# Kernel optimization log

Hardware: AMD Instinct MI355X
Metric: run time of the kernel (lower is better)

Reference implementation:

```python
import math
import jax, jax.numpy as jnp
import numpy as np

B, S, D = 2, 2048, 512
H = 8
DPH = D // H
NEG = -1e18


def lorentz_linear(x, W, b, log_scale):
    """LorentzLinear with head_num=H: linear map then per-head projection onto the
    Lorentz hyperboloid: time = sigmoid(y0)*exp(scale)+1.1, space rescaled so that
    -time^2 + |space|^2 = -1 per head chunk."""
    Bx, Sx, Dx = x.shape
    y = (x @ W.T + b).reshape(Bx, Sx, H, DPH)
    time = jax.nn.sigmoid(y[..., :1]) * jnp.exp(log_scale) + 1.1
    space = y[..., 1:]
    sq = jnp.clip(jnp.sum(space * space, axis=-1, keepdims=True), 1e-8, None)
    scale = (time * time - 1.0) / sq
    out = jnp.concatenate([time, space * jnp.sqrt(scale)], axis=-1)
    return out.reshape(Bx, Sx, Dx)


def setup_inputs() -> dict:
    key0 = jax.random.key(0)
    ks = jax.random.split(key0, 8)
    std = 1.0 / np.sqrt(D)
    causal = ~jnp.tril(jnp.ones((S, S), dtype=bool))  # True = masked out
    return {
        "key": jax.random.normal(ks[0], (B, S, D), jnp.float32),
        "value": jax.random.normal(ks[1], (B, S, D), jnp.float32),
        "query": jax.random.normal(ks[2], (B, S, D), jnp.float32),
        "mask": jnp.broadcast_to(causal[None], (B, S, S)),
        "Wq": jax.random.normal(ks[3], (D, D), jnp.float32) * std,
        "bq": jnp.zeros((D,), jnp.float32),
        "sq": jnp.asarray(math.log(10.0), jnp.float32),
        "Wk": jax.random.normal(ks[4], (D, D), jnp.float32) * std,
        "bk": jnp.zeros((D,), jnp.float32),
        "sk": jnp.asarray(math.log(10.0), jnp.float32),
        "Wv": jax.random.normal(ks[5], (D, D), jnp.float32) * std,
        "bv": jnp.zeros((D,), jnp.float32),
        "sv": jnp.asarray(math.log(10.0), jnp.float32),
        "att_scale": jnp.full((1,), math.sqrt(D), jnp.float32),
        "att_bias": jnp.zeros((), jnp.float32),
    }


def reference(key, value, query, mask, Wq, bq, sq, Wk, bk, sk, Wv, bv, sv,
              att_scale, att_bias):
    def shape(x):  # (B,S,D) -> (B,H,S,dph)
        return x.reshape(B, -1, H, DPH).transpose(0, 2, 1, 3)

    q = shape(lorentz_linear(query, Wq, bq, sq))
    k = shape(lorentz_linear(key, Wk, bk, sk))
    v = shape(lorentz_linear(value, Wv, bv, sv))

    # Lorentz inner product <q,k>_L = -q0*k0 + q_space . k_space
    qm = jnp.concatenate([-q[..., :1], q[..., 1:]], axis=-1)
    cin = jnp.einsum('bhqd,bhkd->bhqk', qm, k)
    scores = (2.0 + 2.0 * cin) / att_scale + att_bias
    scores = jnp.where(mask[:, None], NEG, scores)
    attn = jax.nn.softmax(scores, axis=-1)  # (B,H,Q,K)

    # mid_point: weighted mean then renormalize to the hyperboloid
    ave = jnp.einsum('bhqk,bhkd->bhqd', attn, v)
    inner = -ave[..., :1] ** 2 + jnp.sum(ave[..., 1:] ** 2, axis=-1, keepdims=True)
    denom = jnp.sqrt(jnp.clip(jnp.abs(-inner), 1e-8, None))
    context = (ave / denom).transpose(0, 2, 1, 3)  # (B,Q,H,dph)
    return context, attn
```

## Files before the change

### kernel.cpp

```cpp
#include <hip/hip_runtime.h>
#include <math.h>

#define BB 2
#define SS 2048
#define DD 512
#define HH 8
#define MM (BB*SS)
#define CTX_ELEMS (MM*DD)

typedef __attribute__((ext_vector_type(8))) __bf16 bf16x8;
typedef __attribute__((ext_vector_type(4))) float  f32x4;

static __device__ inline unsigned short f2bf(float x) {
    unsigned u = __builtin_bit_cast(unsigned, x);
    u += 0x7fffu + ((u >> 16) & 1u);
    return (unsigned short)(u >> 16);
}
static __device__ inline float bf2f(unsigned short h) {
    unsigned u = ((unsigned)h) << 16;
    return __builtin_bit_cast(float, u);
}

static __device__ inline void unpack8(const uint4& a, const uint4& b, bf16x8& h, bf16x8& l) {
    uint4 hu, lu;
    hu.x = __builtin_amdgcn_perm(a.y, a.x, 0x05040100u);
    hu.y = __builtin_amdgcn_perm(a.w, a.z, 0x05040100u);
    hu.z = __builtin_amdgcn_perm(b.y, b.x, 0x05040100u);
    hu.w = __builtin_amdgcn_perm(b.w, b.z, 0x05040100u);
    lu.x = __builtin_amdgcn_perm(a.y, a.x, 0x07060302u);
    lu.y = __builtin_amdgcn_perm(a.w, a.z, 0x07060302u);
    lu.z = __builtin_amdgcn_perm(b.y, b.x, 0x07060302u);
    lu.w = __builtin_amdgcn_perm(b.w, b.z, 0x07060302u);
    h = __builtin_bit_cast(bf16x8, hu);
    l = __builtin_bit_cast(bf16x8, lu);
}

__global__ __launch_bounds__(256)
void lorentz_proj_kernel(const float* __restrict__ Xq, const float* __restrict__ Xk, const float* __restrict__ Xv,
                         const float* __restrict__ Wq, const float* __restrict__ bq, const float* __restrict__ sq,
                         const float* __restrict__ Wk, const float* __restrict__ bk, const float* __restrict__ sk,
                         const float* __restrict__ Wv, const float* __restrict__ bv, const float* __restrict__ sv,
                         float* __restrict__ oq, float* __restrict__ ok_, float* __restrict__ ov)
{
    __shared__ float smem[8704];
    float* Xs = smem;
    float* Ws = smem + 4224;

    const float* X; const float* W; const float* bias; const float* ls; float* out;
    if (blockIdx.z == 0)      { X = Xq; W = Wq; bias = bq; ls = sq; out = oq;  }
    else if (blockIdx.z == 1) { X = Xk; W = Wk; bias = bk; ls = sk; out = ok_; }
    else                      { X = Xv; W = Wv; bias = bv; ls = sv; out = ov;  }

    const int tid = threadIdx.x;
    const int tx = tid & 15, ty = tid >> 4;
    const int m0 = blockIdx.x << 7;
    const int n0 = blockIdx.y << 7;

    float acc[8][8];
#pragma unroll
    for (int i = 0; i < 8; ++i)
#pragma unroll
        for (int j = 0; j < 8; ++j) acc[i][j] = 0.f;

    const int lrow = tid >> 3;
    const int lk   = (tid & 7) << 2;

    for (int k0 = 0; k0 < DD; k0 += 32) {
        __syncthreads();
#pragma unroll
        for (int r = 0; r < 4; ++r) {
            const int row = lrow + (r << 5);
            const float4 xv = *(const float4*)(X + (size_t)(m0 + row) * DD + k0 + lk);
            const float4 wv = *(const float4*)(W + (size_t)(n0 + row) * DD + k0 + lk);
            Xs[(lk+0)*132 + row] = xv.x; Xs[(lk+1)*132 + row] = xv.y;
            Xs[(lk+2)*132 + row] = xv.z; Xs[(lk+3)*132 + row] = xv.w;
            Ws[(lk+0)*132 + row] = wv.x; Ws[(lk+1)*132 + row] = wv.y;
            Ws[(lk+2)*132 + row] = wv.z; Ws[(lk+3)*132 + row] = wv.w;
        }
        __syncthreads();
#pragma unroll
        for (int k = 0; k < 32; ++k) {
            const float4 a0 = *(const float4*)(Xs + k*132 + (ty << 3));
            const float4 a1 = *(const float4*)(Xs + k*132 + (ty << 3) + 4);
            const float4 b0 = *(const float4*)(Ws + k*132 + (tx << 3));
            const float4 b1 = *(const float4*)(Ws + k*132 + (tx << 3) + 4);
            const float av[8] = {a0.x,a0.y,a0.z,a0.w,a1.x,a1.y,a1.z,a1.w};
            const float bw[8] = {b0.x,b0.y,b0.z,b0.w,b1.x,b1.y,b1.z,b1.w};
#pragma unroll
            for (int i = 0; i < 8; ++i)
#pragma unroll
                for (int j = 0; j < 8; ++j)
                    acc[i][j] = fmaf(av[i], bw[j], acc[i][j]);
        }
    }

    const float es = expf(ls[0]);

#pragma unroll
    for (int half = 0; half < 2; ++half) {
        __syncthreads();
        if ((tx >> 3) == half) {
            const int cx = tx & 7;
#pragma unroll
            for (int i = 0; i < 8; ++i) {
                const int row = (ty << 3) + i;
#pragma unroll
                for (int j = 0; j < 8; ++j) {
                    const int cih = (cx << 3) + j;
                    smem[row*68 + cih] = acc[i][j] + bias[n0 + (half << 6) + cih];
                }
            }
        }
        __syncthreads();
        const int row = tid >> 1;
        const int t2  = tid & 1;
        float ssum = 0.f;
        for (int j = 1 + t2; j < 64; j += 2) {
            const float v = smem[row*68 + j];
            ssum = fmaf(v, v, ssum);
        }
        ssum += __shfl_xor(ssum, 1);
        const float y0  = smem[row*68];
        const float tim = es / (1.f + expf(-y0)) + 1.1f;
        const float scf = sqrtf((tim*tim - 1.f) / fmaxf(ssum, 1e-8f));
        const int g = m0 + row;
        const int b = g >> 11;
        const int s = g & (SS - 1);
        const int h = (n0 >> 6) + half;
        float* op = out + ((size_t)(b*HH + h)*SS + s) * 64;
        if (t2 == 0) op[0] = tim;
        for (int j = 1 + t2; j < 64; j += 2) op[j] = smem[row*68 + j] * scf;
    }
}

__global__ __launch_bounds__(256)
void lorentz_attn_mfma(const float* __restrict__ qws, const float* __restrict__ kws, const float* __restrict__ vws,
                       const float* __restrict__ att_scale, const float* __restrict__ att_bias,
                       float* __restrict__ ctx, float* __restrict__ attn)
{
    __shared__ __align__(16) char sm[49152];
    char* Kh = sm;
    char* Kl = sm + 8192;
    char* Vp = sm + 16384;
    char* Pp = sm + 32768;
    char* Qh = Pp;
    char* Ql = Pp + 8192;

    const int tid = threadIdx.x;
    const int bh  = blockIdx.y;
    const int qt  = (bh >= 8) ? blockIdx.x : (31 - blockIdx.x);
    const int l63 = tid & 63;
    const int w   = tid >> 6;
    const int qoff = (w >> 1) << 5;
    const int joff = (w & 1) << 5;
    const int lg  = l63 >> 4;
    const int ll  = l63 & 15;

    const float inv_s = 1.f / att_scale[0];
    const float c1 = 2.f * inv_s;
    const float c0 = 2.f * inv_s + att_bias[0];

    const float* qb = qws + (size_t)bh * SS * 64;
    const float* kb = kws + (size_t)bh * SS * 64;
    const float* vb = vws + (size_t)bh * SS * 64;

    const int jr = tid >> 4;
    const int d0 = (tid & 15) << 2;

#pragma unroll
    for (int r = 0; r < 4; ++r) {
        const int j = jr + (r << 4);
        float4 x = *(const float4*)(qb + (size_t)(qt*64 + j)*64 + d0);
        if (d0 == 0) x.x = -x.x;
        const unsigned short h0=f2bf(x.x), h1=f2bf(x.y), h2=f2bf(x.z), h3=f2bf(x.w);
        ushort4 hv = {h0,h1,h2,h3};
        ushort4 lv = {f2bf(x.x-bf2f(h0)), f2bf(x.y-bf2f(h1)), f2bf(x.z-bf2f(h2)), f2bf(x.w-bf2f(h3))};
        const int byte = ((j<<7) + (d0<<1)) ^ ((j&7)<<4);
        *(ushort4*)(Qh + byte) = hv;
        *(ushort4*)(Ql + byte) = lv;
    }
    __syncthreads();

    bf16x8 qh[2][2], ql[2][2];
#pragma unroll
    for (int m = 0; m < 2; ++m)
#pragma unroll
        for (int dc = 0; dc < 2; ++dc) {
            const int q = qoff + (m<<4) + ll;
            const int byte = ((q<<7) + (dc<<6) + (lg<<4)) ^ ((q&7)<<4);
            qh[m][dc] = *(const bf16x8*)(Qh + byte);
            ql[m][dc] = *(const bf16x8*)(Ql + byte);
        }
    __syncthreads();

    float lrow[2][4] = {{0.f,0.f,0.f,0.f},{0.f,0.f,0.f,0.f}};

    for (int jt = 0; jt <= qt; ++jt) {
        __syncthreads();
#pragma unroll
        for (int r = 0; r < 4; ++r) {
            const int j = jr + (r << 4);
            const float4 x = *(const float4*)(kb + (size_t)(jt*64 + j)*64 + d0);
            const unsigned short h0=f2bf(x.x), h1=f2bf(x.y), h2=f2bf(x.z), h3=f2bf(x.w);
            ushort4 hv = {h0,h1,h2,h3};
            ushort4 lv = {f2bf(x.x-bf2f(h0)), f2bf(x.y-bf2f(h1)), f2bf(x.z-bf2f(h2)), f2bf(x.w-bf2f(h3))};
            const int byte = ((j<<7) + (d0<<1)) ^ ((j&7)<<4);
            *(ushort4*)(Kh + byte) = hv;
            *(ushort4*)(Kl + byte) = lv;
        }
        __syncthreads();

        f32x4 sacc[2][2];
#pragma unroll
        for (int m = 0; m < 2; ++m)
#pragma unroll
            for (int n = 0; n < 2; ++n) sacc[m][n] = (f32x4){0.f,0.f,0.f,0.f};
#pragma unroll
        for (int dc = 0; dc < 2; ++dc) {
            bf16x8 kh[2], kl[2];
#pragma unroll
            for (int n = 0; n < 2; ++n) {
                const int j = joff + (n<<4) + ll;
                const int byte = ((j<<7) + (dc<<6) + (lg<<4)) ^ ((j&7)<<4);
                kh[n] = *(const bf16x8*)(Kh + byte);
                kl[n] = *(const bf16x8*)(Kl + byte);
            }
#pragma unroll
            for (int m = 0; m < 2; ++m)
#pragma unroll
                for (int n = 0; n < 2; ++n) {
                    sacc[m][n] = __builtin_amdgcn_mfma_f32_16x16x32_bf16(qh[m][dc], kh[n], sacc[m][n], 0,0,0);
                    sacc[m][n] = __builtin_amdgcn_mfma_f32_16x16x32_bf16(qh[m][dc], kl[n], sacc[m][n], 0,0,0);
                    sacc[m][n] = __builtin_amdgcn_mfma_f32_16x16x32_bf16(ql[m][dc], kh[n], sacc[m][n], 0,0,0);
                }
        }

        const bool diag = (jt == qt);
#pragma unroll
        for (int m = 0; m < 2; ++m)
#pragma unroll
            for (int reg = 0; reg < 4; ++reg) {
                const int ri = qoff + (m<<4) + (lg<<2) + reg;
                float rs = 0.f;
#pragma unroll
                for (int n = 0; n < 2; ++n) {
                    const int cj = joff + (n<<4) + ll;
                    const float sc = sacc[m][n][reg] * c1 + c0;
                    rs += (!diag || cj <= ri) ? __expf(sc) : 0.f;
                }
                rs += __shfl_xor(rs, 1); rs += __shfl_xor(rs, 2);
                rs += __shfl_xor(rs, 4); rs += __shfl_xor(rs, 8);
                lrow[m][reg] += rs;
            }
    }

    __syncthreads();
    {
        float* dred = (float*)sm;
        if (ll == 0) {
#pragma unroll
            for (int m = 0; m < 2; ++m)
#pragma unroll
                for (int reg = 0; reg < 4; ++reg)
                    dred[(qoff + (m<<4) + (lg<<2) + reg)*2 + (w & 1)] = lrow[m][reg];
        }
        __syncthreads();
#pragma unroll
        for (int m = 0; m < 2; ++m)
#pragma unroll
            for (int reg = 0; reg < 4; ++reg) {
                const int ri = qoff + (m<<4) + (lg<<2) + reg;
                lrow[m][reg] = dred[ri*2] + dred[ri*2 + 1];
            }
    }

    float il[2][4];
#pragma unroll
    for (int m = 0; m < 2; ++m)
#pragma unroll
        for (int reg = 0; reg < 4; ++reg) il[m][reg] = 1.f / lrow[m][reg];

    f32x4 oacc[2][2];
#pragma unroll
    for (int m = 0; m < 2; ++m)
#pragma unroll
        for (int n = 0; n < 2; ++n) oacc[m][n] = (f32x4){0.f,0.f,0.f,0.f};

    for (int jt = 0; jt <= qt; ++jt) {
        __syncthreads();
#pragma unroll
        for (int r = 0; r < 4; ++r) {
            const int j = jr + (r << 4);
            const float4 x = *(const float4*)(kb + (size_t)(jt*64 + j)*64 + d0);
            const unsigned short h0=f2bf(x.x), h1=f2bf(x.y), h2=f2bf(x.z), h3=f2bf(x.w);
            ushort4 hv = {h0,h1,h2,h3};
            ushort4 lv = {f2bf(x.x-bf2f(h0)), f2bf(x.y-bf2f(h1)), f2bf(x.z-bf2f(h2)), f2bf(x.w-bf2f(h3))};
            const int byte = ((j<<7) + (d0<<1)) ^ ((j&7)<<4);
            *(ushort4*)(Kh + byte) = hv;
            *(ushort4*)(Kl + byte) = lv;

            const float4 v = *(const float4*)(vb + (size_t)(jt*64 + j)*64 + d0);
            const float vs[4] = {v.x, v.y, v.z, v.w};
#pragma unroll
            for (int c = 0; c < 4; ++c) {
                const int d = d0 + c;
                const unsigned short vh = f2bf(vs[c]);
                const unsigned short vlo = f2bf(vs[c] - bf2f(vh));
                const int vbyte = ((d<<8) + (j<<2)) ^ ((d&7)<<4);
                *(unsigned*)(Vp + vbyte) = (unsigned)vh | ((unsigned)vlo << 16);
            }
        }
        __syncthreads();

        f32x4 sacc[2][2];
#pragma unroll
        for (int m = 0; m < 2; ++m)
#pragma unroll
            for (int n = 0; n < 2; ++n) sacc[m][n] = (f32x4){0.f,0.f,0.f,0.f};
#pragma unroll
        for (int dc = 0; dc < 2; ++dc) {
            bf16x8 kh[2], kl[2];
#pragma unroll
            for (int n = 0; n < 2; ++n) {
                const int j = joff + (n<<4) + ll;
                const int byte = ((j<<7) + (dc<<6) + (lg<<4)) ^ ((j&7)<<4);
                kh[n] = *(const bf16x8*)(Kh + byte);
                kl[n] = *(const bf16x8*)(Kl + byte);
            }
#pragma unroll
            for (int m = 0; m < 2; ++m)
#pragma unroll
                for (int n = 0; n < 2; ++n) {
                    sacc[m][n] = __builtin_amdgcn_mfma_f32_16x16x32_bf16(qh[m][dc], kh[n], sacc[m][n], 0,0,0);
                    sacc[m][n] = __builtin_amdgcn_mfma_f32_16x16x32_bf16(qh[m][dc], kl[n], sacc[m][n], 0,0,0);
                    sacc[m][n] = __builtin_amdgcn_mfma_f32_16x16x32_bf16(ql[m][dc], kh[n], sacc[m][n], 0,0,0);
                }
        }

        const bool diag = (jt == qt);
#pragma unroll
        for (int m = 0; m < 2; ++m)
#pragma unroll
            for (int reg = 0; reg < 4; ++reg) {
                const int ri = qoff + (m<<4) + (lg<<2) + reg;
                const int gi = (qt<<6) + ri;
#pragma unroll
                for (int n = 0; n < 2; ++n) {
                    const int cj = joff + (n<<4) + ll;
                    const float sc = sacc[m][n][reg] * c1 + c0;
                    const float p = (!diag || cj <= ri) ? __expf(sc) : 0.f;
                    const float pn = p * il[m][reg];
                    attn[((size_t)bh*SS + gi)*SS + (jt<<6) + cj] = pn;
                    const unsigned short ph = f2bf(pn);
                    const unsigned short pl = f2bf(pn - bf2f(ph));
                    const int byte = ((ri<<8) + (cj<<2)) ^ ((ri&7)<<4);
                    *(unsigned*)(Pp + byte) = (unsigned)ph | ((unsigned)pl << 16);
                }
            }
        __syncthreads();

#pragma unroll
        for (int jc = 0; jc < 2; ++jc) {
            bf16x8 pah[2], pal[2], vfh[2], vfl[2];
            const int jbase4 = ((jc<<5) + (lg<<3)) << 2;
#pragma unroll
            for (int m = 0; m < 2; ++m) {
                const int q = qoff + (m<<4) + ll;
                const int X = (q<<8) + jbase4;
                const int s = (q&7)<<4;
                const uint4 a = *(const uint4*)(Pp + (X ^ s));
                const uint4 b = *(const uint4*)(Pp + ((X + 16) ^ s));
                unpack8(a, b, pah[m], pal[m]);
            }
#pragma unroll
            for (int n = 0; n < 2; ++n) {
                const int d = joff + (n<<4) + ll;
                const int X = (d<<8) + jbase4;
                const int s = (d&7)<<4;
                const uint4 a = *(const uint4*)(Vp + (X ^ s));
                const uint4 b = *(const uint4*)(Vp + ((X + 16) ^ s));
                unpack8(a, b, vfh[n], vfl[n]);
            }
#pragma unroll
            for (int m = 0; m < 2; ++m)
#pragma unroll
                for (int n = 0; n < 2; ++n) {
                    oacc[m][n] = __builtin_amdgcn_mfma_f32_16x16x32_bf16(pah[m], vfh[n], oacc[m][n], 0,0,0);
                    oacc[m][n] = __builtin_amdgcn_mfma_f32_16x16x32_bf16(pah[m], vfl[n], oacc[m][n], 0,0,0);
                    oacc[m][n] = __builtin_amdgcn_mfma_f32_16x16x32_bf16(pal[m], vfh[n], oacc[m][n], 0,0,0);
                }
        }
    }

    {
        const int cstart = (qt + 1) << 6;
        const float4 z = make_float4(0.f, 0.f, 0.f, 0.f);
        for (int r = 0; r < 64; ++r) {
            float* rowp = attn + ((size_t)bh*SS + (qt<<6) + r)*SS;
            for (int c = cstart + (tid << 2); c < SS; c += 1024)
                *(float4*)(rowp + c) = z;
        }
    }

    float part[2][4];
#pragma unroll
    for (int m = 0; m < 2; ++m)
#pragma unroll
        for (int reg = 0; reg < 4; ++reg) {
            float s = 0.f;
#pragma unroll
            for (int n = 0; n < 2; ++n) {
                const int d = joff + (n<<4) + ll;
                const float av = oacc[m][n][reg] * il[m][reg];
                s += (d == 0) ? -av*av : av*av;
            }
            s += __shfl_xor(s, 1); s += __shfl_xor(s, 2);
            s += __shfl_xor(s, 4); s += __shfl_xor(s, 8);
            part[m][reg] = s;
        }
    __syncthreads();
    float* red = (float*)sm;
    if (ll == 0) {
#pragma unroll
        for (int m = 0; m < 2; ++m)
#pragma unroll
            for (int reg = 0; reg < 4; ++reg)
                red[(qoff + (m<<4) + (lg<<2) + reg)*2 + (w & 1)] = part[m][reg];
    }
    __syncthreads();

    const int b = bh >> 3, h = bh & 7;
#pragma unroll
    for (int m = 0; m < 2; ++m)
#pragma unroll
        for (int reg = 0; reg < 4; ++reg) {
            const int ri = qoff + (m<<4) + (lg<<2) + reg;
            const float inner = red[ri*2] + red[ri*2 + 1];
            const float dinv = 1.f / sqrtf(fmaxf(fabsf(inner), 1e-8f));
            const int gi = (qt<<6) + ri;
#pragma unroll
            for (int n = 0; n < 2; ++n) {
                const int d = joff + (n<<4) + ll;
                const float av = oacc[m][n][reg] * il[m][reg];
                ctx[((size_t)(b*SS + gi)*HH + h)*64 + d] = av * dinv;
            }
        }
}

extern "C" void kernel_launch(void* const* d_in, const int* in_sizes, int n_in,
                              void* d_out, int out_size, void* d_ws, size_t ws_size,
                              hipStream_t stream)
{
    const float* key   = (const float*)d_in[0];
    const float* value = (const float*)d_in[1];
    const float* query = (const float*)d_in[2];
    const float* Wq = (const float*)d_in[4];
    const float* bq = (const float*)d_in[5];
    const float* sq = (const float*)d_in[6];
    const float* Wk = (const float*)d_in[7];
    const float* bk = (const float*)d_in[8];
    const float* sk = (const float*)d_in[9];
    const float* Wv = (const float*)d_in[10];
    const float* bv = (const float*)d_in[11];
    const float* sv = (const float*)d_in[12];
    const float* as_ = (const float*)d_in[13];
    const float* ab  = (const float*)d_in[14];

    float* ws  = (float*)d_ws;
    float* qws = ws;
    float* kws = ws + (size_t)CTX_ELEMS;
    float* vws = ws + (size_t)2 * CTX_ELEMS;

    float* ctx  = (float*)d_out;
    float* attn = ctx + (size_t)CTX_ELEMS;

    dim3 pgrid(MM / 128, DD / 128, 3);
    lorentz_proj_kernel<<<pgrid, 256, 0, stream>>>(query, key, value,
                                                   Wq, bq, sq, Wk, bk, sk, Wv, bv, sv,
                                                   qws, kws, vws);

    dim3 agrid(32, BB * HH);
    lorentz_attn_mfma<<<agrid, 256, 0, stream>>>(qws, kws, vws, as_, ab, ctx, attn);
}
```

Measured before the change: 598.7 us.

## Port Lorentz projection GEMM to bf16x3 MFMA with register-level head normalization

Replaces the FP32 FMA tiled projection GEMM with MFMA 16x16x32 bf16 instructions. Each operand is split into high and low bf16 parts and three products are accumulated to keep near-FP32 accuracy. Tiles are stored in XOR-swizzled shared memory. The hyperboloid normalization epilogue now works directly on the MFMA accumulators, using wave shuffles for the per-head norm instead of a shared-memory staging pass. The tradeoff is extra conversion work, higher shared-memory use (64KB) and a small loss of precision compared with true FP32.

```diff
diff --git a/kernel.cpp b/kernel.cpp
--- a/kernel.cpp
+++ b/kernel.cpp
@@ -36,15 +36,17 @@
 }
 
 __global__ __launch_bounds__(256)
-void lorentz_proj_kernel(const float* __restrict__ Xq, const float* __restrict__ Xk, const float* __restrict__ Xv,
-                         const float* __restrict__ Wq, const float* __restrict__ bq, const float* __restrict__ sq,
-                         const float* __restrict__ Wk, const float* __restrict__ bk, const float* __restrict__ sk,
-                         const float* __restrict__ Wv, const float* __restrict__ bv, const float* __restrict__ sv,
-                         float* __restrict__ oq, float* __restrict__ ok_, float* __restrict__ ov)
+void lorentz_proj_mfma(const float* __restrict__ Xq, const float* __restrict__ Xk, const float* __restrict__ Xv,
+                       const float* __restrict__ Wq, const float* __restrict__ bq, const float* __restrict__ sq,
+                       const float* __restrict__ Wk, const float* __restrict__ bk, const float* __restrict__ sk,
+                       const float* __restrict__ Wv, const float* __restrict__ bv, const float* __restrict__ sv,
+                       float* __restrict__ oq, float* __restrict__ ok_, float* __restrict__ ov)
 {
-    __shared__ float smem[8704];
-    float* Xs = smem;
-    float* Ws = smem + 4224;
+    __shared__ __align__(16) char sm[65536];
+    char* Ah = sm;
+    char* Al = sm + 16384;
+    char* Bh = sm + 32768;
+    char* Bl = sm + 49152;
 
     const float* X; const float* W; const float* bias; const float* ls; float* out;
     if (blockIdx.z == 0)      { X = Xq; W = Wq; bias = bq; ls = sq; out = oq;  }
@@ -52,84 +54,112 @@
     else                      { X = Xv; W = Wv; bias = bv; ls = sv; out = ov;  }
 
     const int tid = threadIdx.x;
-    const int tx = tid & 15, ty = tid >> 4;
+    const int l63 = tid & 63;
+    const int w   = tid >> 6;
+    const int wm  = w >> 1;
+    const int wn  = w & 1;
+    const int lg  = l63 >> 4;
+    const int ll  = l63 & 15;
+
     const int m0 = blockIdx.x << 7;
     const int n0 = blockIdx.y << 7;
 
-    float acc[8][8];
-#pragma unroll
-    for (int i = 0; i < 8; ++i)
-#pragma unroll
-        for (int j = 0; j < 8; ++j) acc[i][j] = 0.f;
-
-    const int lrow = tid >> 3;
-    const int lk   = (tid & 7) << 2;
-
-    for (int k0 = 0; k0 < DD; k0 += 32) {
-        __syncthreads();
-#pragma unroll
-        for (int r = 0; r < 4; ++r) {
-            const int row = lrow + (r << 5);
-            const float4 xv = *(const float4*)(X + (size_t)(m0 + row) * DD + k0 + lk);
-            const float4 wv = *(const float4*)(W + (size_t)(n0 + row) * DD + k0 + lk);
-            Xs[(lk+0)*132 + row] = xv.x; Xs[(lk+1)*132 + row] = xv.y;
-            Xs[(lk+2)*132 + row] = xv.z; Xs[(lk+3)*132 + row] = xv.w;
-            Ws[(lk+0)*132 + row] = wv.x; Ws[(lk+1)*132 + row] = wv.y;
-            Ws[(lk+2)*132 + row] = wv.z; Ws[(lk+3)*132 + row] = wv.w;
-        }
-        __syncthreads();
-#pragma unroll
-        for (int k = 0; k < 32; ++k) {
-            const float4 a0 = *(const float4*)(Xs + k*132 + (ty << 3));
-            const float4 a1 = *(const float4*)(Xs + k*132 + (ty << 3) + 4);
-            const float4 b0 = *(const float4*)(Ws + k*132 + (tx << 3));
-            const float4 b1 = *(const float4*)(Ws + k*132 + (tx << 3) + 4);
-            const float av[8] = {a0.x,a0.y,a0.z,a0.w,a1.x,a1.y,a1.z,a1.w};
-            const float bw[8] = {b0.x,b0.y,b0.z,b0.w,b1.x,b1.y,b1.z,b1.w};
-#pragma unroll
-            for (int i = 0; i < 8; ++i)
-#pragma unroll
-                for (int j = 0; j < 8; ++j)
-                    acc[i][j] = fmaf(av[i], bw[j], acc[i][j]);
+    const int jr = tid >> 4;
+    const int d0 = (tid & 15) << 2;
+
+    f32x4 acc[4][4];
+#pragma unroll
+    for (int m = 0; m < 4; ++m)
+#pragma unroll
+        for (int n = 0; n < 4; ++n) acc[m][n] = (f32x4){0.f,0.f,0.f,0.f};
+
+    for (int k0 = 0; k0 < DD; k0 += 64) {
+        __syncthreads();
+#pragma unroll
+        for (int r = 0; r < 8; ++r) {
+            const int row = jr + (r << 4);
+            const int byte = ((row << 7) + (d0 << 1)) ^ ((row & 7) << 4);
+            {
+                const float4 x = *(const float4*)(X + (size_t)(m0 + row) * DD + k0 + d0);
+                const unsigned short h0=f2bf(x.x), h1=f2bf(x.y), h2=f2bf(x.z), h3=f2bf(x.w);
+                ushort4 hv = {h0,h1,h2,h3};
+                ushort4 lv = {f2bf(x.x-bf2f(h0)), f2bf(x.y-bf2f(h1)), f2bf(x.z-bf2f(h2)), f2bf(x.w-bf2f(h3))};
+                *(ushort4*)(Ah + byte) = hv;
+                *(ushort4*)(Al + byte) = lv;
+            }
+            {
+                const float4 x = *(const float4*)(W + (size_t)(n0 + row) * DD + k0 + d0);
+                const unsigned short h0=f2bf(x.x), h1=f2bf(x.y), h2=f2bf(x.z), h3=f2bf(x.w);
+                ushort4 hv = {h0,h1,h2,h3};
+                ushort4 lv = {f2bf(x.x-bf2f(h0)), f2bf(x.y-bf2f(h1)), f2bf(x.z-bf2f(h2)), f2bf(x.w-bf2f(h3))};
+                *(ushort4*)(Bh + byte) = hv;
+                *(ushort4*)(Bl + byte) = lv;
+            }
+        }
+        __syncthreads();
+
+#pragma unroll
+        for (int dc = 0; dc < 2; ++dc) {
+            bf16x8 ah[4], al4[4], bh[4], bl4[4];
+#pragma unroll
+            for (int m = 0; m < 4; ++m) {
+                const int q = (wm << 6) + (m << 4) + ll;
+                const int byte = ((q << 7) + (dc << 6) + (lg << 4)) ^ ((q & 7) << 4);
+                ah[m]  = *(const bf16x8*)(Ah + byte);
+                al4[m] = *(const bf16x8*)(Al + byte);
+            }
+#pragma unroll
+            for (int n = 0; n < 4; ++n) {
+                const int q = (wn << 6) + (n << 4) + ll;
+                const int byte = ((q << 7) + (dc << 6) + (lg << 4)) ^ ((q & 7) << 4);
+                bh[n]  = *(const bf16x8*)(Bh + byte);
+                bl4[n] = *(const bf16x8*)(Bl + byte);
+            }
+#pragma unroll
+            for (int m = 0; m < 4; ++m)
+#pragma unroll
+                for (int n = 0; n < 4; ++n) {
+                    acc[m][n] = __builtin_amdgcn_mfma_f32_16x16x32_bf16(ah[m],  bh[n],  acc[m][n], 0,0,0);
+                    acc[m][n] = __builtin_amdgcn_mfma_f32_16x16x32_bf16(ah[m],  bl4[n], acc[m][n], 0,0,0);
+                    acc[m][n] = __builtin_amdgcn_mfma_f32_16x16x32_bf16(al4[m], bh[n],  acc[m][n], 0,0,0);
+                }
         }
     }
 
     const float es = expf(ls[0]);
-
-#pragma unroll
-    for (int half = 0; half < 2; ++half) {
-        __syncthreads();
-        if ((tx >> 3) == half) {
-            const int cx = tx & 7;
-#pragma unroll
-            for (int i = 0; i < 8; ++i) {
-                const int row = (ty << 3) + i;
-#pragma unroll
-                for (int j = 0; j < 8; ++j) {
-                    const int cih = (cx << 3) + j;
-                    smem[row*68 + cih] = acc[i][j] + bias[n0 + (half << 6) + cih];
-                }
-            }
-        }
-        __syncthreads();
-        const int row = tid >> 1;
-        const int t2  = tid & 1;
-        float ssum = 0.f;
-        for (int j = 1 + t2; j < 64; j += 2) {
-            const float v = smem[row*68 + j];
-            ssum = fmaf(v, v, ssum);
-        }
-        ssum += __shfl_xor(ssum, 1);
-        const float y0  = smem[row*68];
-        const float tim = es / (1.f + expf(-y0)) + 1.1f;
-        const float scf = sqrtf((tim*tim - 1.f) / fmaxf(ssum, 1e-8f));
-        const int g = m0 + row;
-        const int b = g >> 11;
-        const int s = g & (SS - 1);
-        const int h = (n0 >> 6) + half;
-        float* op = out + ((size_t)(b*HH + h)*SS + s) * 64;
-        if (t2 == 0) op[0] = tim;
-        for (int j = 1 + t2; j < 64; j += 2) op[j] = smem[row*68 + j] * scf;
+    const int h = (blockIdx.y << 1) + wn;
+    float bn[4];
+#pragma unroll
+    for (int n = 0; n < 4; ++n) bn[n] = bias[n0 + (wn << 6) + (n << 4) + ll];
+
+#pragma unroll
+    for (int m = 0; m < 4; ++m) {
+#pragma unroll
+        for (int reg = 0; reg < 4; ++reg) {
+            float y[4];
+            float part = 0.f;
+#pragma unroll
+            for (int n = 0; n < 4; ++n) {
+                y[n] = acc[m][n][reg] + bn[n];
+                const bool is_time = (n == 0) && (ll == 0);
+                part += is_time ? 0.f : y[n]*y[n];
+            }
+            part += __shfl_xor(part, 1); part += __shfl_xor(part, 2);
+            part += __shfl_xor(part, 4); part += __shfl_xor(part, 8);
+            const float y0  = __shfl(y[0], (l63 & 48));
+            const float tim = es / (1.f + expf(-y0)) + 1.1f;
+            const float scf = sqrtf((tim*tim - 1.f) / fmaxf(part, 1e-8f));
+
+            const int gr = m0 + (wm << 6) + (m << 4) + (lg << 2) + reg;
+            const int b  = gr >> 11;
+            const int s  = gr & (SS - 1);
+            float* op = out + ((size_t)(b*HH + h)*SS + s) * 64;
+#pragma unroll
+            for (int n = 0; n < 4; ++n) {
+                const int cih = (n << 4) + ll;
+                op[cih] = (cih == 0) ? tim : y[n] * scf;
+            }
+        }
     }
 }
 
@@ -475,9 +505,9 @@
     float* attn = ctx + (size_t)CTX_ELEMS;
 
     dim3 pgrid(MM / 128, DD / 128, 3);
-    lorentz_proj_kernel<<<pgrid, 256, 0, stream>>>(query, key, value,
-                                                   Wq, bq, sq, Wk, bk, sk, Wv, bv, sv,
-                                                   qws, kws, vws);
+    lorentz_proj_mfma<<<pgrid, 256, 0, stream>>>(query, key, value,
+                                                 Wq, bq, sq, Wk, bk, sk, Wv, bv, sv,
+                                                 qws, kws, vws);
 
     dim3 agrid(32, BB * HH);
     lorentz_attn_mfma<<<agrid, 256, 0, stream>>>(qws, kws, vws, as_, ab, ctx, attn);
```

Result: faster. 558.4 us (-6.7%).
